# Performance work log

Measured on AMD Instinct MI355X. Metric: run time of the kernel, lower is better.

## Reference

```python
import jax, jax.numpy as jnp
import numpy as np

BSZ, L, D_INNER, D_STATE = 2, 2048, 2048, 8
DT_RANK = D_INNER // 8  # 256


def setup_inputs() -> dict:
    key = jax.random.key(0)
    k0, k1, k2, k3 = jax.random.split(key, 4)
    x = jax.random.normal(k0, (BSZ, L, D_INNER), jnp.float32)
    # x_proj: Linear(d_inner -> dt_rank + 2*d_state), no bias
    W_xproj = jax.random.normal(k1, (DT_RANK + 2 * D_STATE, D_INNER), jnp.float32) * 0.02
    # dt_proj: Linear(dt_rank -> d_inner), uniform(-dt_rank^-0.5, +)
    std = DT_RANK ** -0.5
    W_dt = jax.random.uniform(k2, (D_INNER, DT_RANK), jnp.float32, -std, std)
    # dt bias init: inverse-softplus of dt ~ LogUniform(1e-3, 1e-1)
    dt = jnp.exp(jax.random.uniform(k3, (D_INNER,), jnp.float32)
                 * (jnp.log(0.1) - jnp.log(0.001)) + jnp.log(0.001))
    dt = jnp.clip(dt, 1e-4)
    b_dt = dt + jnp.log(-jnp.expm1(-dt))
    # A = repeat(arange(1, N+1), 'n -> d n'); A_log = log(A)
    A_log = jnp.log(jnp.broadcast_to(
        jnp.arange(1, D_STATE + 1, dtype=jnp.float32), (D_INNER, D_STATE)))
    D_param = jnp.ones((D_INNER,), jnp.float32)
    return {"x": x, "W_xproj": W_xproj, "W_dt": W_dt, "b_dt": b_dt,
            "A_log": A_log, "D_param": D_param}


def reference(x, W_xproj, W_dt, b_dt, A_log, D_param):
    # x: (B, L, D)
    d_state = A_log.shape[1]
    dt_rank = W_dt.shape[1]
    x_dbl = jnp.einsum('bld,kd->blk', x, W_xproj)          # (B,L,dt_rank+2N)
    dt_r = x_dbl[..., :dt_rank]
    B_ssm = x_dbl[..., dt_rank:dt_rank + d_state]          # (B,L,N)
    C_ssm = x_dbl[..., dt_rank + d_state:]                 # (B,L,N)
    delta = jax.nn.softplus(jnp.einsum('blr,dr->bld', dt_r, W_dt) + b_dt)  # (B,L,D) > 0
    A = -jnp.exp(A_log)                                     # (D,N) < 0
    # Discretization: dA = exp(delta*A), dBu = delta*B*u
    dA = jnp.exp(delta[..., None] * A)                      # (B,L,D,N)
    dBu = (delta * x)[..., None] * B_ssm[:, :, None, :]     # (B,L,D,N)

    # Linear recurrence h_t = dA_t * h_{t-1} + dBu_t via associative scan over L
    def combine(c1, c2):
        a1, b1 = c1
        a2, b2 = c2
        return a1 * a2, a2 * b1 + b2

    _, h = jax.lax.associative_scan(combine, (dA, dBu), axis=1)  # (B,L,D,N)
    y = jnp.einsum('bldn,bln->bld', h, C_ssm) + x * D_param
    return y
```

## Files before the change

### kernel.cpp

```cpp
#include <hip/hip_runtime.h>
#include <math.h>

#define BSZ    2
#define LSEQ   2048
#define DI     2048
#define DSTATE 8
#define DTRANK 256
#define KXP    (DTRANK + 2 * DSTATE)
#define NPAD   288
#define NC     64
#define CL     (LSEQ / NC)
#define KSPLIT 8
#define KCHUNK (DI / KSPLIT)

#define NWXP (288u * 2048u)
#define NWX  (272u * 2048u)
#define NWDT (2048u * 256u)

typedef __attribute__((ext_vector_type(8))) short bf16x8;
typedef __attribute__((ext_vector_type(4))) float f32x4;

static __device__ __forceinline__ unsigned short f2bf(float f) {
    unsigned u = __float_as_uint(f);
    u += 0x7fff + ((u >> 16) & 1);
    return (unsigned short)(u >> 16);
}
static __device__ __forceinline__ float bf2f(unsigned short s) {
    return __uint_as_float((unsigned)s << 16);
}

static __device__ __forceinline__ float softplus_fast(float z) {
    const float e = __expf(-fabsf(z));
    return fmaxf(z, 0.0f) + __logf(1.0f + e);
}

__global__ __launch_bounds__(256) void convert_w(const float* __restrict__ Wx,
                                                 const float* __restrict__ Wdt,
                                                 unsigned short* __restrict__ Wxb,
                                                 unsigned short* __restrict__ Wdtb) {
    const unsigned tid = blockIdx.x * 256 + threadIdx.x;
    const unsigned i4 = tid * 4;
    float4 v;
    unsigned short* dst;
    unsigned j;
    if (i4 < NWXP) {
        j = i4;
        v = (j < NWX) ? *(const float4*)&Wx[j] : make_float4(0.f, 0.f, 0.f, 0.f);
        dst = Wxb;
    } else {
        j = i4 - NWXP;
        if (j >= NWDT) return;
        v = *(const float4*)&Wdt[j];
        dst = Wdtb;
    }
    ushort4 o;
    o.x = f2bf(v.x); o.y = f2bf(v.y); o.z = f2bf(v.z); o.w = f2bf(v.w);
    *(ushort4*)&dst[j] = o;
}

#define G1RS 40
__global__ __launch_bounds__(256) void gemm1_mfma(const float* __restrict__ x,
                                                  const unsigned short* __restrict__ Wxb,
                                                  unsigned short* __restrict__ partb) {
    __shared__ __align__(16) unsigned short As[64 * G1RS];
    __shared__ __align__(16) unsigned short Bs[288 * G1RS];
    const int mt   = blockIdx.x;
    const int ks   = blockIdx.y;
    const int t    = threadIdx.x;
    const int wave = t >> 6;
    const int lane = t & 63;
    const int quad = lane >> 4;
    const int r    = lane & 15;
    const int rh   = wave >> 1;
    const int nh   = wave & 1;
    const int m0   = mt * 64;

    const int arow = t >> 2;
    const int aoff = (t & 3) * 8;

    f32x4 acc[2][9];
#pragma unroll
    for (int f = 0; f < 2; f++)
#pragma unroll
        for (int n = 0; n < 9; n++) acc[f][n] = (f32x4)(0.0f);

    const int kbeg = ks * KCHUNK;
    for (int k0 = kbeg; k0 < kbeg + KCHUNK; k0 += 32) {
        const float4 a0 = *(const float4*)&x[(size_t)(m0 + arow) * DI + k0 + aoff];
        const float4 a1 = *(const float4*)&x[(size_t)(m0 + arow) * DI + k0 + aoff + 4];
        bf16x8 bstage[5];
#pragma unroll
        for (int j = 0; j < 5; j++) {
            const int i = t + j * 256;
            if (i < 1152)
                bstage[j] = *(const bf16x8*)&Wxb[(size_t)(i >> 2) * DI + k0 + (i & 3) * 8];
        }
        __syncthreads();
        bf16x8 av;
        av[0] = (short)f2bf(a0.x); av[1] = (short)f2bf(a0.y);
        av[2] = (short)f2bf(a0.z); av[3] = (short)f2bf(a0.w);
        av[4] = (short)f2bf(a1.x); av[5] = (short)f2bf(a1.y);
        av[6] = (short)f2bf(a1.z); av[7] = (short)f2bf(a1.w);
        *(bf16x8*)&As[arow * G1RS + aoff] = av;
#pragma unroll
        for (int j = 0; j < 5; j++) {
            const int i = t + j * 256;
            if (i < 1152)
                *(bf16x8*)&Bs[(i >> 2) * G1RS + (i & 3) * 8] = bstage[j];
        }
        __syncthreads();

        bf16x8 af[2], bf[9];
#pragma unroll
        for (int f = 0; f < 2; f++)
            af[f] = *(const bf16x8*)&As[(rh * 32 + f * 16 + r) * G1RS + quad * 8];
#pragma unroll
        for (int nf = 0; nf < 9; nf++)
            bf[nf] = *(const bf16x8*)&Bs[(nh * 144 + nf * 16 + r) * G1RS + quad * 8];
#pragma unroll
        for (int f = 0; f < 2; f++)
#pragma unroll
            for (int nf = 0; nf < 9; nf++)
                acc[f][nf] = __builtin_amdgcn_mfma_f32_16x16x32_bf16(af[f], bf[nf], acc[f][nf], 0, 0, 0);
    }

    unsigned short* p = partb + (size_t)ks * 4096 * NPAD;
#pragma unroll
    for (int f = 0; f < 2; f++) {
        const int row0 = m0 + rh * 32 + f * 16 + quad * 4;
#pragma unroll
        for (int nf = 0; nf < 9; nf++) {
            const int col = nh * 144 + nf * 16 + r;
#pragma unroll
            for (int i = 0; i < 4; i++)
                p[(size_t)(row0 + i) * NPAD + col] = f2bf(acc[f][nf][i]);
        }
    }
}

__global__ __launch_bounds__(256) void reduce1(const unsigned short* __restrict__ partb,
                                               float* __restrict__ xdbl,
                                               unsigned short* __restrict__ dtr) {
    const int tid = blockIdx.x * 256 + threadIdx.x;
    const int row = tid / 72;
    const int c4  = (tid - row * 72) * 4;
    float4 s = make_float4(0.f, 0.f, 0.f, 0.f);
#pragma unroll
    for (int ks = 0; ks < KSPLIT; ks++) {
        const ushort4 v = *(const ushort4*)&partb[(size_t)ks * 4096 * NPAD + (size_t)row * NPAD + c4];
        s.x += bf2f(v.x); s.y += bf2f(v.y); s.z += bf2f(v.z); s.w += bf2f(v.w);
    }
    if (c4 < KXP) *(float4*)&xdbl[(size_t)row * KXP + c4] = s;
    if (c4 < DTRANK) {
        ushort4 o;
        o.x = f2bf(s.x); o.y = f2bf(s.y); o.z = f2bf(s.z); o.w = f2bf(s.w);
        *(ushort4*)&dtr[(size_t)row * DTRANK + c4] = o;
    }
}

#define G2RS 40
__global__ __launch_bounds__(256, 2) void gemm2_mfma(const unsigned short* __restrict__ dtr,
                                                     const unsigned short* __restrict__ Wdtb,
                                                     const float* __restrict__ bdt,
                                                     float* __restrict__ delta) {
    __shared__ __align__(16) unsigned short As[128 * G2RS];
    __shared__ __align__(16) unsigned short Bs[128 * G2RS];
    const int nt   = blockIdx.x;
    const int mt   = blockIdx.y;
    const int t    = threadIdx.x;
    const int wave = t >> 6;
    const int lane = t & 63;
    const int quad = lane >> 4;
    const int r    = lane & 15;
    const int m0 = mt * 128, n0 = nt * 128;
    const int mw = (wave >> 1) * 64, nw = (wave & 1) * 64;

    const int srow = t >> 1;
    const int sc   = (t & 1) * 16;

    f32x4 acc[4][4];
#pragma unroll
    for (int f = 0; f < 4; f++)
#pragma unroll
        for (int g = 0; g < 4; g++) acc[f][g] = (f32x4)(0.0f);

    for (int k0 = 0; k0 < DTRANK; k0 += 32) {
        const bf16x8 a0 = *(const bf16x8*)&dtr[(size_t)(m0 + srow) * DTRANK + k0 + sc];
        const bf16x8 a1 = *(const bf16x8*)&dtr[(size_t)(m0 + srow) * DTRANK + k0 + sc + 8];
        const bf16x8 b0 = *(const bf16x8*)&Wdtb[(size_t)(n0 + srow) * DTRANK + k0 + sc];
        const bf16x8 b1 = *(const bf16x8*)&Wdtb[(size_t)(n0 + srow) * DTRANK + k0 + sc + 8];
        __syncthreads();
        *(bf16x8*)&As[srow * G2RS + sc]     = a0;
        *(bf16x8*)&As[srow * G2RS + sc + 8] = a1;
        *(bf16x8*)&Bs[srow * G2RS + sc]     = b0;
        *(bf16x8*)&Bs[srow * G2RS + sc + 8] = b1;
        __syncthreads();

        bf16x8 a[4], b[4];
#pragma unroll
        for (int f = 0; f < 4; f++)
            a[f] = *(const bf16x8*)&As[(mw + f * 16 + r) * G2RS + quad * 8];
#pragma unroll
        for (int g = 0; g < 4; g++)
            b[g] = *(const bf16x8*)&Bs[(nw + g * 16 + r) * G2RS + quad * 8];
#pragma unroll
        for (int f = 0; f < 4; f++)
#pragma unroll
            for (int g = 0; g < 4; g++)
                acc[f][g] = __builtin_amdgcn_mfma_f32_16x16x32_bf16(a[f], b[g], acc[f][g], 0, 0, 0);
    }

#pragma unroll
    for (int f = 0; f < 4; f++) {
        const int row0 = m0 + mw + f * 16 + quad * 4;
#pragma unroll
        for (int g = 0; g < 4; g++) {
            const int col = n0 + nw + g * 16 + r;
            const float bv = bdt[col];
#pragma unroll
            for (int i = 0; i < 4; i++)
                delta[(size_t)(row0 + i) * DI + col] = softplus_fast(acc[f][g][i] + bv);
        }
    }
}

__global__ __launch_bounds__(256) void scan_pass1(const float* __restrict__ x,
                                                  const float* __restrict__ delta,
                                                  const float* __restrict__ xdbl,
                                                  const float* __restrict__ Alog,
                                                  float* __restrict__ Pb,
                                                  float* __restrict__ Hb) {
    __shared__ __align__(16) float Ls[CL * 8];
    const int bi   = blockIdx.x;
    const int b    = bi >> 9;
    const int c    = (bi >> 3) & 63;
    const int dblk = bi & 7;
    const int d    = dblk * 256 + threadIdx.x;
    const int l0   = c * CL;
    const size_t row0 = (size_t)b * LSEQ + l0;

    if (threadIdx.x < CL * 2) {
        const int l = threadIdx.x >> 1, part = (threadIdx.x & 1) * 4;
        const float4 v = *(const float4*)&xdbl[(row0 + l) * KXP + DTRANK + part];
        *(float4*)&Ls[l * 8 + part] = v;
    }

    float A[8], h[8], P[8];
#pragma unroll
    for (int n = 0; n < 8; n++) {
        A[n] = -__expf(Alog[d * 8 + n]);
        h[n] = 0.f;
        P[n] = 1.f;
    }
    __syncthreads();

#pragma unroll 4
    for (int l = 0; l < CL; l++) {
        const size_t row = row0 + l;
        const float dl = delta[row * DI + d];
        const float xv = x[row * DI + d];
        const float du = dl * xv;
#pragma unroll
        for (int n = 0; n < 8; n++) {
            const float dA = __expf(dl * A[n]);
            h[n] = dA * h[n] + du * Ls[l * 8 + n];
            P[n] *= dA;
        }
    }
    const size_t base = ((size_t)(b * NC + c) * DI + d) * 8;
    *(float4*)&Pb[base]     = make_float4(P[0], P[1], P[2], P[3]);
    *(float4*)&Pb[base + 4] = make_float4(P[4], P[5], P[6], P[7]);
    *(float4*)&Hb[base]     = make_float4(h[0], h[1], h[2], h[3]);
    *(float4*)&Hb[base + 4] = make_float4(h[4], h[5], h[6], h[7]);
}

__global__ __launch_bounds__(256) void scan_pass2(const float* __restrict__ Pb,
                                                  const float* __restrict__ Hb,
                                                  float* __restrict__ h0) {
    const int t   = blockIdx.x * 256 + threadIdx.x;
    const int b   = t >> 14;
    const int rem = t & 16383;
    float h = 0.f;
#pragma unroll 4
    for (int c = 0; c < NC; c++) {
        const size_t base = (size_t)(b * NC + c) * (DI * 8) + rem;
        h0[base] = h;
        h = Pb[base] * h + Hb[base];
    }
}

__global__ __launch_bounds__(256) void scan_pass3(const float* __restrict__ x,
                                                  const float* __restrict__ delta,
                                                  const float* __restrict__ xdbl,
                                                  const float* __restrict__ Alog,
                                                  const float* __restrict__ Dp,
                                                  const float* __restrict__ h0,
                                                  float* __restrict__ y) {
    __shared__ __align__(16) float Ls[CL * 16];
    const int bi   = blockIdx.x;
    const int b    = bi >> 9;
    const int c    = (bi >> 3) & 63;
    const int dblk = bi & 7;
    const int d    = dblk * 256 + threadIdx.x;
    const int l0   = c * CL;
    const size_t row0 = (size_t)b * LSEQ + l0;

    if (threadIdx.x < CL * 4) {
        const int l = threadIdx.x >> 2, part = (threadIdx.x & 3) * 4;
        const float4 v = *(const float4*)&xdbl[(row0 + l) * KXP + DTRANK + part];
        *(float4*)&Ls[l * 16 + part] = v;
    }

    float A[8], h[8];
    const size_t hbase = ((size_t)(b * NC + c) * DI + d) * 8;
    const float4 h0a = *(const float4*)&h0[hbase];
    const float4 h0b = *(const float4*)&h0[hbase + 4];
    h[0] = h0a.x; h[1] = h0a.y; h[2] = h0a.z; h[3] = h0a.w;
    h[4] = h0b.x; h[5] = h0b.y; h[6] = h0b.z; h[7] = h0b.w;
#pragma unroll
    for (int n = 0; n < 8; n++) A[n] = -__expf(Alog[d * 8 + n]);
    const float Dpar = Dp[d];
    __syncthreads();

#pragma unroll 4
    for (int l = 0; l < CL; l++) {
        const size_t row = row0 + l;
        const float dl = delta[row * DI + d];
        const float xv = x[row * DI + d];
        const float du = dl * xv;
        float yv = 0.f;
#pragma unroll
        for (int n = 0; n < 8; n++) {
            const float dA = __expf(dl * A[n]);
            h[n] = dA * h[n] + du * Ls[l * 16 + n];
            yv += h[n] * Ls[l * 16 + 8 + n];
        }
        yv += xv * Dpar;
        y[row * DI + d] = yv;
    }
}

extern "C" void kernel_launch(void* const* d_in, const int* in_sizes, int n_in,
                              void* d_out, int out_size, void* d_ws, size_t ws_size,
                              hipStream_t stream) {
    const float* x    = (const float*)d_in[0];
    const float* Wx   = (const float*)d_in[1];
    const float* Wdt  = (const float*)d_in[2];
    const float* bdt  = (const float*)d_in[3];
    const float* Alog = (const float*)d_in[4];
    const float* Dp   = (const float*)d_in[5];
    float* y = (float*)d_out;

    float* ws    = (float*)d_ws;
    unsigned short* partb = (unsigned short*)ws;
    float* delta = ws;
    float* xdbl  = ws + 8388608;
    float* Pb    = xdbl + 1114112;
    float* Hb    = Pb + 2097152;
    float* h0    = Hb + 2097152;
    unsigned short* Wxb  = (unsigned short*)(h0 + 2097152);
    unsigned short* Wdtb = Wxb + (size_t)NWXP;
    unsigned short* dtr  = Wdtb + (size_t)NWDT;

    dim3 blk(256);
    hipLaunchKernelGGL(convert_w, dim3((NWXP + NWDT) / 4 / 256), blk, 0, stream,
                       Wx, Wdt, Wxb, Wdtb);
    hipLaunchKernelGGL(gemm1_mfma, dim3(64, KSPLIT), blk, 0, stream, x, Wxb, partb);
    hipLaunchKernelGGL(reduce1, dim3(4096 * 72 / 256), blk, 0, stream, partb, xdbl, dtr);
    hipLaunchKernelGGL(gemm2_mfma, dim3(16, 32), blk, 0, stream, dtr, Wdtb, bdt, delta);
    hipLaunchKernelGGL(scan_pass1, dim3(BSZ * NC * 8), blk, 0, stream, x, delta, xdbl, Alog, Pb, Hb);
    hipLaunchKernelGGL(scan_pass2, dim3(128), blk, 0, stream, Pb, Hb, h0);
    hipLaunchKernelGGL(scan_pass3, dim3(BSZ * NC * 8), blk, 0, stream, x, delta, xdbl, Alog, Dp, h0, y);
}
```

Before: 181.8 us.

## Fuse three scan passes into one cooperative kernel and store delta as bf16

The three scan kernels (chunk summaries, cross-chunk carry, final output) become one cooperative kernel separated by grid-wide syncs, which removes two launches and keeps the B/C tiles in shared memory across phases. Delta is now written and read as bf16, halving its memory traffic, and B/C are packed into a compact 16-wide buffer. The cost is the overhead of grid syncs, a cooperative-launch requirement that all 1024 blocks be co-resident, and reduced precision in delta.

```diff
diff --git a/kernel.cpp b/kernel.cpp
--- a/kernel.cpp
+++ b/kernel.cpp
@@ -1,5 +1,8 @@
 #include <hip/hip_runtime.h>
+#include <hip/hip_cooperative_groups.h>
 #include <math.h>
+
+namespace cg = cooperative_groups;
 
 #define BSZ    2
 #define LSEQ   2048
@@ -12,6 +15,7 @@
 #define CL     (LSEQ / NC)
 #define KSPLIT 8
 #define KCHUNK (DI / KSPLIT)
+#define SCAN_BLOCKS (BSZ * NC * 8)
 
 #define NWXP (288u * 2048u)
 #define NWX  (272u * 2048u)
@@ -139,8 +143,8 @@
 }
 
 __global__ __launch_bounds__(256) void reduce1(const unsigned short* __restrict__ partb,
-                                               float* __restrict__ xdbl,
-                                               unsigned short* __restrict__ dtr) {
+                                               unsigned short* __restrict__ dtr,
+                                               float* __restrict__ BC) {
     const int tid = blockIdx.x * 256 + threadIdx.x;
     const int row = tid / 72;
     const int c4  = (tid - row * 72) * 4;
@@ -150,11 +154,12 @@
         const ushort4 v = *(const ushort4*)&partb[(size_t)ks * 4096 * NPAD + (size_t)row * NPAD + c4];
         s.x += bf2f(v.x); s.y += bf2f(v.y); s.z += bf2f(v.z); s.w += bf2f(v.w);
     }
-    if (c4 < KXP) *(float4*)&xdbl[(size_t)row * KXP + c4] = s;
     if (c4 < DTRANK) {
         ushort4 o;
         o.x = f2bf(s.x); o.y = f2bf(s.y); o.z = f2bf(s.z); o.w = f2bf(s.w);
         *(ushort4*)&dtr[(size_t)row * DTRANK + c4] = o;
+    } else if (c4 < KXP) {
+        *(float4*)&BC[(size_t)row * 16 + (c4 - DTRANK)] = s;
     }
 }
 
@@ -162,7 +167,7 @@
 __global__ __launch_bounds__(256, 2) void gemm2_mfma(const unsigned short* __restrict__ dtr,
                                                      const unsigned short* __restrict__ Wdtb,
                                                      const float* __restrict__ bdt,
-                                                     float* __restrict__ delta) {
+                                                     unsigned short* __restrict__ deltab) {
     __shared__ __align__(16) unsigned short As[128 * G2RS];
     __shared__ __align__(16) unsigned short Bs[128 * G2RS];
     const int nt   = blockIdx.x;
@@ -219,113 +224,88 @@
             const float bv = bdt[col];
 #pragma unroll
             for (int i = 0; i < 4; i++)
-                delta[(size_t)(row0 + i) * DI + col] = softplus_fast(acc[f][g][i] + bv);
-        }
-    }
-}
-
-__global__ __launch_bounds__(256) void scan_pass1(const float* __restrict__ x,
-                                                  const float* __restrict__ delta,
-                                                  const float* __restrict__ xdbl,
-                                                  const float* __restrict__ Alog,
-                                                  float* __restrict__ Pb,
-                                                  float* __restrict__ Hb) {
-    __shared__ __align__(16) float Ls[CL * 8];
-    const int bi   = blockIdx.x;
-    const int b    = bi >> 9;
-    const int c    = (bi >> 3) & 63;
-    const int dblk = bi & 7;
-    const int d    = dblk * 256 + threadIdx.x;
-    const int l0   = c * CL;
-    const size_t row0 = (size_t)b * LSEQ + l0;
-
-    if (threadIdx.x < CL * 2) {
-        const int l = threadIdx.x >> 1, part = (threadIdx.x & 1) * 4;
-        const float4 v = *(const float4*)&xdbl[(row0 + l) * KXP + DTRANK + part];
-        *(float4*)&Ls[l * 8 + part] = v;
-    }
-
-    float A[8], h[8], P[8];
-#pragma unroll
-    for (int n = 0; n < 8; n++) {
-        A[n] = -__expf(Alog[d * 8 + n]);
-        h[n] = 0.f;
-        P[n] = 1.f;
-    }
-    __syncthreads();
-
-#pragma unroll 4
-    for (int l = 0; l < CL; l++) {
-        const size_t row = row0 + l;
-        const float dl = delta[row * DI + d];
-        const float xv = x[row * DI + d];
-        const float du = dl * xv;
-#pragma unroll
-        for (int n = 0; n < 8; n++) {
-            const float dA = __expf(dl * A[n]);
-            h[n] = dA * h[n] + du * Ls[l * 8 + n];
-            P[n] *= dA;
-        }
-    }
-    const size_t base = ((size_t)(b * NC + c) * DI + d) * 8;
-    *(float4*)&Pb[base]     = make_float4(P[0], P[1], P[2], P[3]);
-    *(float4*)&Pb[base + 4] = make_float4(P[4], P[5], P[6], P[7]);
-    *(float4*)&Hb[base]     = make_float4(h[0], h[1], h[2], h[3]);
-    *(float4*)&Hb[base + 4] = make_float4(h[4], h[5], h[6], h[7]);
-}
-
-__global__ __launch_bounds__(256) void scan_pass2(const float* __restrict__ Pb,
-                                                  const float* __restrict__ Hb,
-                                                  float* __restrict__ h0) {
-    const int t   = blockIdx.x * 256 + threadIdx.x;
-    const int b   = t >> 14;
-    const int rem = t & 16383;
-    float h = 0.f;
-#pragma unroll 4
-    for (int c = 0; c < NC; c++) {
-        const size_t base = (size_t)(b * NC + c) * (DI * 8) + rem;
-        h0[base] = h;
-        h = Pb[base] * h + Hb[base];
-    }
-}
-
-__global__ __launch_bounds__(256) void scan_pass3(const float* __restrict__ x,
-                                                  const float* __restrict__ delta,
-                                                  const float* __restrict__ xdbl,
-                                                  const float* __restrict__ Alog,
-                                                  const float* __restrict__ Dp,
-                                                  const float* __restrict__ h0,
-                                                  float* __restrict__ y) {
+                deltab[(size_t)(row0 + i) * DI + col] = f2bf(softplus_fast(acc[f][g][i] + bv));
+        }
+    }
+}
+
+__global__ __launch_bounds__(256, 4) void scan_fused(const float* __restrict__ x,
+                                                     const unsigned short* __restrict__ deltab,
+                                                     const float* __restrict__ BC,
+                                                     const float* __restrict__ Alog,
+                                                     const float* __restrict__ Dp,
+                                                     float* __restrict__ Pb,
+                                                     float* __restrict__ Hb,
+                                                     float* __restrict__ h0,
+                                                     float* __restrict__ y) {
     __shared__ __align__(16) float Ls[CL * 16];
     const int bi   = blockIdx.x;
     const int b    = bi >> 9;
     const int c    = (bi >> 3) & 63;
     const int dblk = bi & 7;
-    const int d    = dblk * 256 + threadIdx.x;
+    const int tid  = threadIdx.x;
+    const int d    = dblk * 256 + tid;
     const int l0   = c * CL;
     const size_t row0 = (size_t)b * LSEQ + l0;
 
-    if (threadIdx.x < CL * 4) {
-        const int l = threadIdx.x >> 2, part = (threadIdx.x & 3) * 4;
-        const float4 v = *(const float4*)&xdbl[(row0 + l) * KXP + DTRANK + part];
-        *(float4*)&Ls[l * 16 + part] = v;
-    }
-
-    float A[8], h[8];
-    const size_t hbase = ((size_t)(b * NC + c) * DI + d) * 8;
-    const float4 h0a = *(const float4*)&h0[hbase];
-    const float4 h0b = *(const float4*)&h0[hbase + 4];
+    if (tid < CL * 4) {
+        const int l = tid >> 2, part = (tid & 3) * 4;
+        *(float4*)&Ls[l * 16 + part] = *(const float4*)&BC[(row0 + l) * 16 + part];
+    }
+
+    float A[8], P[8], H[8];
+#pragma unroll
+    for (int n = 0; n < 8; n++) {
+        A[n] = -__expf(Alog[d * 8 + n]);
+        P[n] = 1.f;
+        H[n] = 0.f;
+    }
+    __syncthreads();
+
+    for (int l = 0; l < CL; l++) {
+        const size_t row = row0 + l;
+        const float dl = bf2f(deltab[row * DI + d]);
+        const float xv = x[row * DI + d];
+        const float du = dl * xv;
+#pragma unroll
+        for (int n = 0; n < 8; n++) {
+            const float dA = __expf(dl * A[n]);
+            H[n] = dA * H[n] + du * Ls[l * 16 + n];
+            P[n] *= dA;
+        }
+    }
+    const size_t base = ((size_t)(b * NC + c) * DI + d) * 8;
+    *(float4*)&Pb[base]     = make_float4(P[0], P[1], P[2], P[3]);
+    *(float4*)&Pb[base + 4] = make_float4(P[4], P[5], P[6], P[7]);
+    *(float4*)&Hb[base]     = make_float4(H[0], H[1], H[2], H[3]);
+    *(float4*)&Hb[base + 4] = make_float4(H[4], H[5], H[6], H[7]);
+
+    cg::this_grid().sync();
+
+    const int gt = bi * 256 + tid;
+    if (gt < BSZ * DI * 8) {
+        const int b2  = gt >> 14;
+        const int rem = gt & 16383;
+        float h = 0.f;
+        for (int cc = 0; cc < NC; cc++) {
+            const size_t bb = (size_t)(b2 * NC + cc) * (DI * 8) + rem;
+            h0[bb] = h;
+            h = Pb[bb] * h + Hb[bb];
+        }
+    }
+
+    cg::this_grid().sync();
+
+    float h[8];
+    const float4 h0a = *(const float4*)&h0[base];
+    const float4 h0b = *(const float4*)&h0[base + 4];
     h[0] = h0a.x; h[1] = h0a.y; h[2] = h0a.z; h[3] = h0a.w;
     h[4] = h0b.x; h[5] = h0b.y; h[6] = h0b.z; h[7] = h0b.w;
-#pragma unroll
-    for (int n = 0; n < 8; n++) A[n] = -__expf(Alog[d * 8 + n]);
     const float Dpar = Dp[d];
-    __syncthreads();
-
-#pragma unroll 4
+
     for (int l = 0; l < CL; l++) {
         const size_t row = row0 + l;
-        const float dl = delta[row * DI + d];
+        const float dl = bf2f(deltab[row * DI + d]);
         const float xv = x[row * DI + d];
         const float du = dl * xv;
         float yv = 0.f;
@@ -335,8 +315,7 @@
             h[n] = dA * h[n] + du * Ls[l * 16 + n];
             yv += h[n] * Ls[l * 16 + 8 + n];
         }
-        yv += xv * Dpar;
-        y[row * DI + d] = yv;
+        y[row * DI + d] = yv + xv * Dpar;
     }
 }
 
@@ -351,24 +330,27 @@
     const float* Dp   = (const float*)d_in[5];
     float* y = (float*)d_out;
 
-    float* ws    = (float*)d_ws;
-    unsigned short* partb = (unsigned short*)ws;
-    float* delta = ws;
-    float* xdbl  = ws + 8388608;
-    float* Pb    = xdbl + 1114112;
-    float* Hb    = Pb + 2097152;
-    float* h0    = Hb + 2097152;
-    unsigned short* Wxb  = (unsigned short*)(h0 + 2097152);
-    unsigned short* Wdtb = Wxb + (size_t)NWXP;
-    unsigned short* dtr  = Wdtb + (size_t)NWDT;
+    float* ws = (float*)d_ws;
+    unsigned short* partb  = (unsigned short*)ws;
+    unsigned short* deltab = (unsigned short*)ws;
+    float* BC = ws + 4718592;
+    float* Pb = ws + 4784128;
+    float* Hb = ws + 6881280;
+    float* h0 = ws + 8978432;
+    unsigned short* Wxb  = (unsigned short*)(ws + 11075584);
+    unsigned short* Wdtb = (unsigned short*)(ws + 11370496);
+    unsigned short* dtr  = (unsigned short*)(ws + 11632640);
 
     dim3 blk(256);
     hipLaunchKernelGGL(convert_w, dim3((NWXP + NWDT) / 4 / 256), blk, 0, stream,
                        Wx, Wdt, Wxb, Wdtb);
     hipLaunchKernelGGL(gemm1_mfma, dim3(64, KSPLIT), blk, 0, stream, x, Wxb, partb);
-    hipLaunchKernelGGL(reduce1, dim3(4096 * 72 / 256), blk, 0, stream, partb, xdbl, dtr);
-    hipLaunchKernelGGL(gemm2_mfma, dim3(16, 32), blk, 0, stream, dtr, Wdtb, bdt, delta);
-    hipLaunchKernelGGL(scan_pass1, dim3(BSZ * NC * 8), blk, 0, stream, x, delta, xdbl, Alog, Pb, Hb);
-    hipLaunchKernelGGL(scan_pass2, dim3(128), blk, 0, stream, Pb, Hb, h0);
-    hipLaunchKernelGGL(scan_pass3, dim3(BSZ * NC * 8), blk, 0, stream, x, delta, xdbl, Alog, Dp, h0, y);
-}
+    hipLaunchKernelGGL(reduce1, dim3(4096 * 72 / 256), blk, 0, stream, partb, dtr, BC);
+    hipLaunchKernelGGL(gemm2_mfma, dim3(16, 32), blk, 0, stream, dtr, Wdtb, bdt, deltab);
+
+    const unsigned short* deltab_c = deltab;
+    const float* BC_c = BC;
+    void* args[] = {(void*)&x, (void*)&deltab_c, (void*)&BC_c, (void*)&Alog, (void*)&Dp,
+                    (void*)&Pb, (void*)&Hb, (void*)&h0, (void*)&y};
+    hipLaunchCooperativeKernel((void*)scan_fused, dim3(SCAN_BLOCKS), blk, args, 0, stream);
+}
```

Result: slower. 428.3 us (+135.6%).
